# Kernel tuning notes

Hardware: AMD Instinct MI355X
Metric: run time of the kernel (lower is better)

Reference implementation:

```python
import jax, jax.numpy as jnp
import numpy as np

NS = 50000   # number of source cells
NT = 50000   # number of target cells
E = 1_600_000  # nnz of neighborhood (avg degree 32)
DIN = 64
DOUT = 64


def setup_inputs() -> dict:
    key = jax.random.key(0)
    ks = jax.random.split(key, 14)
    w_scale = ((2.0 / (DIN + DOUT)) ** 0.5) * 1.414  # xavier_uniform-ish std with gain
    a_scale = (1.0 / (3 * DOUT)) ** 0.5
    nrm = lambda k, s, sc: jax.random.normal(k, s, jnp.float32) * sc
    return {
        "x_source": jax.random.normal(ks[0], (NS, DIN), jnp.float32),
        "x_target": jax.random.normal(ks[1], (NT, DIN), jnp.float32),
        "nb_rows": jax.random.randint(ks[2], (E,), 0, NT, jnp.int32),   # target index of each nnz
        "nb_cols": jax.random.randint(ks[3], (E,), 0, NS, jnp.int32),   # source index of each nnz
        "nb_vals": jax.random.uniform(ks[4], (E,), jnp.float32),        # neighborhood values
        "cci_vals": jax.random.uniform(ks[5], (E,), jnp.float32),       # cci values (same pattern)
        "w_s": nrm(ks[6], (DIN, DOUT), w_scale),
        "w_t": nrm(ks[7], (DIN, DOUT), w_scale),
        "w_s_cci": nrm(ks[8], (DIN, DOUT), w_scale),   # shared: ParameterList([p]*2) aliases one param
        "w_t_cci": nrm(ks[9], (DIN, DOUT), w_scale),
        "src_W": nrm(ks[10], (3, 3 * DOUT, DOUT), a_scale),
        "src_b": jnp.zeros((3, DOUT), jnp.float32),
        "tgt_W": nrm(ks[11], (3, 3 * DOUT, DOUT), a_scale),
        "tgt_b": jnp.zeros((3, DOUT), jnp.float32),
    }


def _pna(seg, nbr, vals, m, W, b, n_seg):
    """PNA aggregation over a sparse neighborhood given as an edge list.
    seg: [E] destination segment ids; nbr: [E] neighbor ids into m; vals: [E] edge weights.
    Aggregators: weighted sum, mean (by neighbor count), max; then Linear(3D -> D)."""
    g = m[nbr] * vals[:, None]                                   # [E, D]
    s_sum = jax.ops.segment_sum(g, seg, num_segments=n_seg)      # [n_seg, D]
    cnt = jax.ops.segment_sum(jnp.ones_like(vals), seg, num_segments=n_seg)
    s_mean = s_sum / jnp.maximum(cnt, 1.0)[:, None]
    s_max = jax.ops.segment_max(g, seg, num_segments=n_seg)
    s_max = jnp.where(jnp.isfinite(s_max), s_max, 0.0)           # empty segments -> 0
    return jnp.concatenate([s_sum, s_mean, s_max], axis=-1) @ W + b


def reference(x_source, x_target, nb_rows, nb_cols, nb_vals, cci_vals,
              w_s, w_t, w_s_cci, w_t_cci, src_W, src_b, tgt_W, tgt_b):
    n_s, n_t = x_source.shape[0], x_target.shape[0]
    # dense projections (w_s_cci / w_t_cci are shared between the two cci branches)
    s_msg = x_source @ w_s          # [NS, DOUT]
    s_msg2 = x_source @ w_s_cci     # used for both cci branches
    t_msg = x_target @ w_t          # [NT, DOUT]
    t_msg2 = x_target @ w_t_cci
    had_vals = cci_vals * nb_vals   # sparse hadamard (same pattern)

    # message on source: aggregate target features along transposed neighborhood [NS, NT]
    msg_src = (_pna(nb_cols, nb_rows, nb_vals, t_msg, src_W[0], src_b[0], n_s)
               + _pna(nb_cols, nb_rows, cci_vals, t_msg2, src_W[1], src_b[1], n_s)
               + _pna(nb_cols, nb_rows, had_vals, t_msg2, src_W[2], src_b[2], n_s))
    # message on target: aggregate source features along neighborhood [NT, NS]
    msg_tgt = (_pna(nb_rows, nb_cols, nb_vals, s_msg, tgt_W[0], tgt_b[0], n_t)
               + _pna(nb_rows, nb_cols, cci_vals, s_msg2, tgt_W[1], tgt_b[1], n_t)
               + _pna(nb_rows, nb_cols, had_vals, s_msg2, tgt_W[2], tgt_b[2], n_t))
    # update_func is None -> return raw messages
    return msg_src, msg_tgt
```

## Files before the change

kernel.cpp:

```cpp
#include <hip/hip_runtime.h>
#include <hip/hip_bf16.h>

typedef unsigned int u32;
typedef unsigned short u16;
typedef unsigned long long u64;
typedef __attribute__((ext_vector_type(8))) short short8;
typedef __attribute__((ext_vector_type(4))) float f32x4;

__device__ __forceinline__ u32 f2bf(float f){
  u32 u = __float_as_uint(f);
  return (u + 0x7fffu + ((u >> 16) & 1u)) >> 16;
}
__device__ __forceinline__ float bflo(u32 p){ return __uint_as_float(p << 16); }
__device__ __forceinline__ float bfhi(u32 p){ return __uint_as_float(p & 0xffff0000u); }

__global__ __launch_bounds__(256) void proj_kernel(
    const float* __restrict__ xs, const float* __restrict__ xt,
    const float* __restrict__ w_s, const float* __restrict__ w_t,
    const float* __restrict__ w_s_cci, const float* __restrict__ w_t_cci,
    u32* __restrict__ mS, u32* __restrict__ mT, int ns, int nt)
{
  __shared__ float wa[4096], wb[4096];
  const int dir = blockIdx.y;
  const float* x  = dir ? xt : xs;
  const float* wA = dir ? w_t : w_s;
  const float* wB = dir ? w_t_cci : w_s_cci;
  u32* out = dir ? mT : mS;
  const int n = dir ? nt : ns;
  const int tid = threadIdx.x;
  for (int i = tid; i < 4096; i += 256){ wa[i] = wA[i]; wb[i] = wB[i]; }
  __syncthreads();
  const int wid = tid >> 6, lane = tid & 63;
  const int slice = lane >> 4, ch = lane & 15;
  for (int row = blockIdx.x*4 + wid; row < n; row += gridDim.x*4){
    float xv = x[(size_t)row*64 + lane];
    float accA = 0.f, accB = 0.f;
    #pragma unroll
    for (int k = 0; k < 64; k++){
      float xk = __shfl(xv, k, 64);
      accA = fmaf(xk, wa[k*64 + lane], accA);
      accB = fmaf(xk, wb[k*64 + lane], accB);
    }
    out[((size_t)slice*n + row)*16 + ch] = f2bf(accA) | (f2bf(accB) << 16);
  }
}

__global__ __launch_bounds__(256) void wprep_kernel(
  const float* __restrict__ srcW, const float* __restrict__ tgtW,
  u16* __restrict__ WtS, u16* __restrict__ WtT)
{
  int idx = blockIdx.x*256 + threadIdx.x;
  if (idx < 576*64){
    int col = idx / 576, k = idx - col*576;
    WtS[idx] = (u16)f2bf(srcW[(size_t)k*64 + col]);
    WtT[idx] = (u16)f2bf(tgtW[(size_t)k*64 + col]);
  }
}

__global__ __launch_bounds__(256) void hist_kernel(
  const int* __restrict__ rows, const int* __restrict__ cols,
  int* cntR, int* cntC, int E)
{
  int e = blockIdx.x*256 + threadIdx.x;
  if (e < E){
    atomicAdd(&cntR[rows[e]], 1);
    atomicAdd(&cntC[cols[e]], 1);
  }
}

__global__ __launch_bounds__(256) void scan1_kernel(
  const int* __restrict__ cntC, const int* __restrict__ cntR,
  int* __restrict__ locC, int* __restrict__ locR,
  int* __restrict__ bsum, int ns, int nt)
{
  const int arr = blockIdx.y;
  const int* cnt = arr ? cntR : cntC;
  int* loc = arr ? locR : locC;
  const int n = arr ? nt : ns;
  const int base = blockIdx.x*1024 + threadIdx.x*4;
  int v[4]; int s = 0;
  #pragma unroll
  for (int i = 0; i < 4; i++){ int idx = base+i; v[i] = (idx < n) ? cnt[idx] : 0; s += v[i]; }
  const int lane = threadIdx.x & 63, wid = threadIdx.x >> 6;
  int ps = s;
  #pragma unroll
  for (int d = 1; d < 64; d <<= 1){ int t = __shfl_up(ps, d, 64); if (lane >= d) ps += t; }
  __shared__ int wsum[4];
  if (lane == 63) wsum[wid] = ps;
  __syncthreads();
  int woff = 0;
  for (int w = 0; w < wid; w++) woff += wsum[w];
  int ex = woff + ps - s;
  #pragma unroll
  for (int i = 0; i < 4; i++){ int idx = base+i; if (idx < n) loc[idx] = ex; ex += v[i]; }
  if (threadIdx.x == 255) bsum[arr*64 + blockIdx.x] = woff + ps;
}

__global__ __launch_bounds__(128) void scan2_kernel(
  int* __restrict__ bsum, int* __restrict__ ptrC, int* __restrict__ ptrR,
  int ns, int nt)
{
  const int wid = threadIdx.x >> 6, lane = threadIdx.x & 63;
  const int n = wid ? nt : ns;
  const int nb = (n + 1023) >> 10;
  int v = (lane < nb) ? bsum[wid*64 + lane] : 0;
  int ps = v;
  #pragma unroll
  for (int d = 1; d < 64; d <<= 1){ int t = __shfl_up(ps, d, 64); if (lane >= d) ps += t; }
  if (lane < nb) bsum[wid*64 + lane] = ps - v;
  if (lane == 63){ if (wid) ptrR[nt] = ps; else ptrC[ns] = ps; }
}

__global__ __launch_bounds__(256) void scan3_kernel(
  const int* __restrict__ locC, const int* __restrict__ locR,
  const int* __restrict__ bsum,
  int* __restrict__ ptrC, int* __restrict__ ptrR,
  int* __restrict__ curC, int* __restrict__ curR, int ns, int nt)
{
  const int arr = blockIdx.y;
  const int* loc = arr ? locR : locC;
  int* ptr = arr ? ptrR : ptrC;
  int* cur = arr ? curR : curC;
  const int n = arr ? nt : ns;
  const int off = bsum[arr*64 + blockIdx.x];
  const int base = blockIdx.x*1024 + threadIdx.x;
  #pragma unroll
  for (int i = 0; i < 4; i++){
    int idx = base + i*256;
    if (idx < n){ int p = loc[idx] + off; ptr[idx] = p; cur[idx] = p; }
  }
}

__global__ __launch_bounds__(256) void scatter_kernel(
  const int* __restrict__ rows, const int* __restrict__ cols,
  const float* __restrict__ nbv, const float* __restrict__ ccv,
  int* curR, int* curC,
  int* nbrT, float* w0T, float* w1T,
  int* nbrS, float* w0S, float* w1S, int E)
{
  int e = blockIdx.x*256 + threadIdx.x;
  if (e < E){
    int r = rows[e], c = cols[e];
    float a = nbv[e], b = ccv[e];
    int pT = atomicAdd(&curR[r], 1);
    nbrT[pT] = c; w0T[pT] = a; w1T[pT] = b;
    int pS = atomicAdd(&curC[c], 1);
    nbrS[pS] = r; w0S[pS] = a; w1S[pS] = b;
  }
}

__global__ __launch_bounds__(256) void repack_kernel(
  const int* __restrict__ nbrT, const float* __restrict__ w0T, const float* __restrict__ w1T,
  const int* __restrict__ nbrS, const float* __restrict__ w0S, const float* __restrict__ w1S,
  u64* __restrict__ recT, u64* __restrict__ recS, int E)
{
  int e = blockIdx.x*256 + threadIdx.x;
  if (e < E){
    {
      float a = w0T[e], b = w1T[e];
      recT[e] = (u64)(u16)nbrT[e] | ((u64)f2bf(a) << 16) | ((u64)f2bf(b) << 32)
              | ((u64)f2bf(a*b) << 48);
    }
    {
      float a = w0S[e], b = w1S[e];
      recS[e] = (u64)(u16)nbrS[e] | ((u64)f2bf(a) << 16) | ((u64)f2bf(b) << 32)
              | ((u64)f2bf(a*b) << 48);
    }
  }
}

__global__ __launch_bounds__(256) void agg_kernel(
  const int* __restrict__ ptrC, const int* __restrict__ ptrR,
  const u64* __restrict__ recS, const u64* __restrict__ recT,
  const u32* __restrict__ mS, const u32* __restrict__ mT,
  u16* __restrict__ statsS, u16* __restrict__ statsT, int ns, int nt)
{
  const int z = blockIdx.z;
  const int dir = z >> 2, slice = z & 3;
  const int nseg = dir ? nt : ns;
  const int ntab = dir ? ns : nt;
  const int* ptr = dir ? ptrR : ptrC;
  const u64* rec = dir ? recT : recS;
  const u32* mtab = (dir ? mS : mT) + (size_t)slice*ntab*16;
  u16* stats = dir ? statsT : statsS;

  const int wid = threadIdx.x >> 6, lane = threadIdx.x & 63;
  const int seg = blockIdx.x*4 + wid;
  if (seg >= nseg) return;
  const int beg = ptr[seg], end = ptr[seg+1];
  const u32 egrp = (u32)(lane >> 4);
  const u32 chb = (u32)((lane & 15) << 2);

  float s0=0.f, s1=0.f, s2=0.f;
  float mx0=-INFINITY, mx1=-INFINITY, mx2=-INFINITY;

  const int cnt = end - beg;
  const u32 nq = (u32)(cnt >> 2);
  const u32 r  = (u32)(cnt & 3);
  u32 e = (u32)beg + egrp;

  #define GREC(i)   (rec[(size_t)(u32)(i)])
  #define GFT(p)    (*(const u32*)((const char*)mtab + (size_t)(((u32)(p) & 0xffffu)*64u + chb)))
  #define CONSUME(p, f) { \
    u32 lo_ = (u32)(p), hi_ = (u32)((p) >> 32); \
    float a_ = bfhi(lo_), b_ = bflo(hi_), ab_ = bfhi(hi_); \
    float tl_ = bflo(f), th_ = bfhi(f); \
    float g0_ = tl_*a_, g1_ = th_*b_, g2_ = th_*ab_; \
    s0 += g0_; s1 += g1_; s2 += g2_; \
    mx0 = fmaxf(mx0, g0_); mx1 = fmaxf(mx1, g1_); mx2 = fmaxf(mx2, g2_); }

  u32 k = 0;
  if (nq >= 8){
    u64 p0 = GREC(e),    p1 = GREC(e+4),  p2 = GREC(e+8),  p3 = GREC(e+12);
    u32 f0 = GFT(p0),    f1 = GFT(p1),    f2 = GFT(p2),    f3 = GFT(p3);
    u64 q0 = GREC(e+16), q1 = GREC(e+20), q2 = GREC(e+24), q3 = GREC(e+28);
    for (; k + 12 <= nq; k += 4, e += 16){
      u64 r0 = GREC(e+32), r1 = GREC(e+36), r2 = GREC(e+40), r3 = GREC(e+44);
      u32 g0 = GFT(q0), g1 = GFT(q1), g2 = GFT(q2), g3 = GFT(q3);
      CONSUME(p0, f0); CONSUME(p1, f1); CONSUME(p2, f2); CONSUME(p3, f3);
      p0=q0; p1=q1; p2=q2; p3=q3;
      f0=g0; f1=g1; f2=g2; f3=g3;
      q0=r0; q1=r1; q2=r2; q3=r3;
    }
    u32 g0 = GFT(q0), g1 = GFT(q1), g2 = GFT(q2), g3 = GFT(q3);
    CONSUME(p0, f0); CONSUME(p1, f1); CONSUME(p2, f2); CONSUME(p3, f3);
    CONSUME(q0, g0); CONSUME(q1, g1); CONSUME(q2, g2); CONSUME(q3, g3);
    k += 8; e += 32;
  }
  for (; k < nq; k++, e += 4){
    u64 p = GREC(e);
    u32 f = GFT(p);
    CONSUME(p, f);
  }
  if (egrp < r){
    u64 p = GREC((u32)beg + 4*nq + egrp);
    u32 f = GFT(p);
    CONSUME(p, f);
  }
  #undef GREC
  #undef GFT
  #undef CONSUME

  #pragma unroll
  for (int d = 16; d <= 32; d <<= 1){
    s0 += __shfl_xor(s0, d, 64);
    s1 += __shfl_xor(s1, d, 64);
    s2 += __shfl_xor(s2, d, 64);
    mx0 = fmaxf(mx0, __shfl_xor(mx0, d, 64));
    mx1 = fmaxf(mx1, __shfl_xor(mx1, d, 64));
    mx2 = fmaxf(mx2, __shfl_xor(mx2, d, 64));
  }
  if (cnt == 0){ mx0 = 0.f; mx1 = 0.f; mx2 = 0.f; }

  if (lane < 16){
    size_t base = ((size_t)slice*nseg + seg)*96 + (lane & 15);
    stats[base      ] = (u16)f2bf(s0);
    stats[base + 16 ] = (u16)f2bf(s1);
    stats[base + 32 ] = (u16)f2bf(s2);
    stats[base + 48 ] = (u16)f2bf(mx0);
    stats[base + 64 ] = (u16)f2bf(mx1);
    stats[base + 80 ] = (u16)f2bf(mx2);
  }
}

#define HROW 584

__global__ __launch_bounds__(256) void lin_kernel(
  const u16* __restrict__ statsS, const u16* __restrict__ statsT,
  const int* __restrict__ ptrC, const int* __restrict__ ptrR,
  const u16* __restrict__ WtS, const u16* __restrict__ WtT,
  const float* __restrict__ srcB, const float* __restrict__ tgtB,
  float* __restrict__ outp, int ns, int nt)
{
  __shared__ u16 h[64*HROW];
  __shared__ float invc[64];
  const int dir = blockIdx.y;
  const u16* stats = dir ? statsT : statsS;
  const int* ptr   = dir ? ptrR : ptrC;
  const u16* Wt    = dir ? WtT : WtS;
  const float* Bg  = dir ? tgtB : srcB;
  const int n = dir ? nt : ns;
  float* out = outp + (dir ? (size_t)ns*64 : 0);
  const int tid = threadIdx.x;
  const int wv = tid >> 6, lane = tid & 63;
  const int seg0 = blockIdx.x * 64;
  if (seg0 >= n) return;

  const int bcol = wv*16 + (lane & 15);
  const int krow = (lane >> 4) * 8;
  short8 bfrag[18];
  #pragma unroll
  for (int t = 0; t < 18; t++)
    bfrag[t] = *(const short8*)&Wt[(size_t)bcol*576 + t*32 + krow];

  if (tid < 64){
    int seg = seg0 + tid;
    float c = (seg < n) ? (float)(ptr[seg+1] - ptr[seg]) : 1.f;
    invc[tid] = 1.f / fmaxf(c, 1.f);
  }
  __syncthreads();

  for (int idx = tid; idx < 64*192; idx += 256){
    int s = idx / 192, i = idx - s*192;
    int blk = i >> 5, cp = (i & 31) * 2;
    int seg = seg0 + s;
    u32 v = 0;
    if (seg < n)
      v = *(const u32*)&stats[((size_t)(cp >> 4)*n + seg)*96 + blk*16 + (cp & 15)];
    u32* hrow = (u32*)&h[s*HROW];
    if (blk < 3){
      hrow[(blk*192 + cp) >> 1] = v;
      float ic = invc[s];
      hrow[(blk*192 + 64 + cp) >> 1] = f2bf(bflo(v)*ic) | (f2bf(bfhi(v)*ic) << 16);
    } else {
      hrow[((blk-3)*192 + 128 + cp) >> 1] = v;
    }
  }
  __syncthreads();

  f32x4 acc[4] = {};
  const int arow = lane & 15;
  #pragma unroll
  for (int t = 0; t < 18; t++){
    #pragma unroll
    for (int rb = 0; rb < 4; rb++){
      short8 a = *(const short8*)&h[(rb*16 + arow)*HROW + t*32 + krow];
      acc[rb] = __builtin_amdgcn_mfma_f32_16x16x32_bf16(a, bfrag[t], acc[rb], 0, 0, 0);
    }
  }

  float bv = Bg[bcol] + Bg[64 + bcol] + Bg[128 + bcol];
  #pragma unroll
  for (int rb = 0; rb < 4; rb++){
    #pragma unroll
    for (int r = 0; r < 4; r++){
      int seg = seg0 + rb*16 + (lane >> 4)*4 + r;
      if (seg < n) out[(size_t)seg*64 + bcol] = acc[rb][r] + bv;
    }
  }
}

extern "C" void kernel_launch(void* const* d_in, const int* in_sizes, int n_in,
                              void* d_out, int out_size, void* d_ws, size_t ws_size,
                              hipStream_t stream)
{
  const float* xs   = (const float*)d_in[0];
  const float* xt   = (const float*)d_in[1];
  const int*   rows = (const int*)  d_in[2];
  const int*   cols = (const int*)  d_in[3];
  const float* nbv  = (const float*)d_in[4];
  const float* ccv  = (const float*)d_in[5];
  const float* w_s  = (const float*)d_in[6];
  const float* w_t  = (const float*)d_in[7];
  const float* w_sc = (const float*)d_in[8];
  const float* w_tc = (const float*)d_in[9];
  const float* srcW = (const float*)d_in[10];
  const float* srcB = (const float*)d_in[11];
  const float* tgtW = (const float*)d_in[12];
  const float* tgtB = (const float*)d_in[13];
  const int ns = in_sizes[0] / 64;
  const int nt = in_sizes[1] / 64;
  const int E  = in_sizes[4];

  char* ws = (char*)d_ws;
  size_t off = 0;
  auto alloc = [&](size_t bytes)->char* {
    char* p = ws + off;
    off = (off + bytes + 255) & ~(size_t)255;
    return p;
  };
  u32* mS    = (u32*)alloc((size_t)ns*64*4);
  u32* mT    = (u32*)alloc((size_t)nt*64*4);
  int* cntC  = (int*)alloc((size_t)(ns+nt)*4);
  int* cntR  = cntC + ns;
  int* ptrC  = (int*)alloc((size_t)(ns+1)*4);
  int* ptrR  = (int*)alloc((size_t)(nt+1)*4);
  int* curC  = (int*)alloc((size_t)ns*4);
  int* curR  = (int*)alloc((size_t)nt*4);
  int* locC  = (int*)alloc((size_t)ns*4);
  int* locR  = (int*)alloc((size_t)nt*4);
  int* bsum  = (int*)alloc((size_t)128*4);
  int*   nbrS = (int*)  alloc((size_t)E*4);
  float* w0S  = (float*)alloc((size_t)E*4);
  float* w1S  = (float*)alloc((size_t)E*4);
  int*   nbrT = (int*)  alloc((size_t)E*4);
  float* w0T  = (float*)alloc((size_t)E*4);
  float* w1T  = (float*)alloc((size_t)E*4);
  u64* recS   = (u64*)alloc((size_t)E*8);
  u64* recT   = (u64*)alloc((size_t)E*8);
  u16* statsS = (u16*)alloc((size_t)ns*384*2);
  u16* statsT = (u16*)alloc((size_t)nt*384*2);
  u16* WtS    = (u16*)alloc((size_t)576*64*2);
  u16* WtT    = (u16*)alloc((size_t)576*64*2);

  const int mseg = (ns > nt ? ns : nt);
  const int nsb = (mseg + 1023) / 1024;

  hipMemsetAsync(cntC, 0, (size_t)(ns+nt)*4, stream);
  proj_kernel<<<dim3(128,2), 256, 0, stream>>>(xs,xt,w_s,w_t,w_sc,w_tc,mS,mT,ns,nt);
  wprep_kernel<<<(576*64 + 255)/256, 256, 0, stream>>>(srcW,tgtW,WtS,WtT);
  hist_kernel<<<(E+255)/256, 256, 0, stream>>>(rows,cols,cntR,cntC,E);
  scan1_kernel<<<dim3(nsb,2), 256, 0, stream>>>(cntC,cntR,locC,locR,bsum,ns,nt);
  scan2_kernel<<<1, 128, 0, stream>>>(bsum,ptrC,ptrR,ns,nt);
  scan3_kernel<<<dim3(nsb,2), 256, 0, stream>>>(locC,locR,bsum,ptrC,ptrR,curC,curR,ns,nt);
  scatter_kernel<<<(E+255)/256, 256, 0, stream>>>(rows,cols,nbv,ccv,curR,curC,
                                                  nbrT,w0T,w1T,nbrS,w0S,w1S,E);
  repack_kernel<<<(E+255)/256, 256, 0, stream>>>(nbrT,w0T,w1T,nbrS,w0S,w1S,
                                                 recT,recS,E);
  agg_kernel<<<dim3((mseg+3)/4, 1, 8), 256, 0, stream>>>(ptrC,ptrR,recS,recT,
                                                         mS,mT,statsS,statsT,ns,nt);
  lin_kernel<<<dim3((mseg+63)/64, 2), 256, 0, stream>>>(statsS,statsT,ptrC,ptrR,
                                                        WtS,WtT,srcB,tgtB,
                                                        (float*)d_out,ns,nt);
}
```

Measured before the change: 875.6 us.

## Merge preprocessing kernels, single-pass decoupled-lookback scan, split and simplify aggregation

Folds the weight-transpose prep into the histogram kernel and replaces the three-kernel scan with one decoupled-lookback scan that uses flag words in a zeroed state buffer. The scatter kernel now handles two edges per thread, and the aggregation kernel is split into one launch per direction, with a simpler 8-wide unrolled loop in place of the software-pipelined one. The aim is fewer launches and less intermediate traffic. The trade-offs are spin-waiting between blocks in the scan and possibly less latency hiding in the aggregation loop.

```diff
diff --git a/kernel.cpp b/kernel.cpp
--- a/kernel.cpp
+++ b/kernel.cpp
@@ -45,39 +45,41 @@
   }
 }
 
-__global__ __launch_bounds__(256) void wprep_kernel(
+__global__ __launch_bounds__(256) void hist_kernel(
+  const int* __restrict__ rows, const int* __restrict__ cols,
+  int* cntR, int* cntC, int E,
   const float* __restrict__ srcW, const float* __restrict__ tgtW,
   u16* __restrict__ WtS, u16* __restrict__ WtT)
-{
-  int idx = blockIdx.x*256 + threadIdx.x;
-  if (idx < 576*64){
-    int col = idx / 576, k = idx - col*576;
-    WtS[idx] = (u16)f2bf(srcW[(size_t)k*64 + col]);
-    WtT[idx] = (u16)f2bf(tgtW[(size_t)k*64 + col]);
-  }
-}
-
-__global__ __launch_bounds__(256) void hist_kernel(
-  const int* __restrict__ rows, const int* __restrict__ cols,
-  int* cntR, int* cntC, int E)
 {
   int e = blockIdx.x*256 + threadIdx.x;
   if (e < E){
     atomicAdd(&cntR[rows[e]], 1);
     atomicAdd(&cntC[cols[e]], 1);
   }
-}
-
-__global__ __launch_bounds__(256) void scan1_kernel(
+  if (e < 576*64){
+    int col = e / 576, k = e - col*576;
+    WtS[e] = (u16)f2bf(srcW[(size_t)k*64 + col]);
+    WtT[e] = (u16)f2bf(tgtW[(size_t)k*64 + col]);
+  }
+}
+
+__global__ __launch_bounds__(256) void scan_kernel(
   const int* __restrict__ cntC, const int* __restrict__ cntR,
-  int* __restrict__ locC, int* __restrict__ locR,
-  int* __restrict__ bsum, int ns, int nt)
+  int* __restrict__ ptrC, int* __restrict__ ptrR,
+  int* __restrict__ curC, int* __restrict__ curR,
+  u64* __restrict__ state, int ns, int nt)
 {
   const int arr = blockIdx.y;
   const int* cnt = arr ? cntR : cntC;
-  int* loc = arr ? locR : locC;
+  int* ptr = arr ? ptrR : ptrC;
+  int* cur = arr ? curR : curC;
   const int n = arr ? nt : ns;
-  const int base = blockIdx.x*1024 + threadIdx.x*4;
+  const int nb = (n + 1023) >> 10;
+  const int b = blockIdx.x;
+  if (b >= nb) return;
+  u64* st = state + arr*64;
+
+  const int base = b*1024 + threadIdx.x*4;
   int v[4]; int s = 0;
   #pragma unroll
   for (int i = 0; i < 4; i++){ int idx = base+i; v[i] = (idx < n) ? cnt[idx] : 0; s += v[i]; }
@@ -86,48 +88,40 @@
   #pragma unroll
   for (int d = 1; d < 64; d <<= 1){ int t = __shfl_up(ps, d, 64); if (lane >= d) ps += t; }
   __shared__ int wsum[4];
+  __shared__ int bloff;
   if (lane == 63) wsum[wid] = ps;
   __syncthreads();
   int woff = 0;
   for (int w = 0; w < wid; w++) woff += wsum[w];
-  int ex = woff + ps - s;
-  #pragma unroll
-  for (int i = 0; i < 4; i++){ int idx = base+i; if (idx < n) loc[idx] = ex; ex += v[i]; }
-  if (threadIdx.x == 255) bsum[arr*64 + blockIdx.x] = woff + ps;
-}
-
-__global__ __launch_bounds__(128) void scan2_kernel(
-  int* __restrict__ bsum, int* __restrict__ ptrC, int* __restrict__ ptrR,
-  int ns, int nt)
-{
-  const int wid = threadIdx.x >> 6, lane = threadIdx.x & 63;
-  const int n = wid ? nt : ns;
-  const int nb = (n + 1023) >> 10;
-  int v = (lane < nb) ? bsum[wid*64 + lane] : 0;
-  int ps = v;
-  #pragma unroll
-  for (int d = 1; d < 64; d <<= 1){ int t = __shfl_up(ps, d, 64); if (lane >= d) ps += t; }
-  if (lane < nb) bsum[wid*64 + lane] = ps - v;
-  if (lane == 63){ if (wid) ptrR[nt] = ps; else ptrC[ns] = ps; }
-}
-
-__global__ __launch_bounds__(256) void scan3_kernel(
-  const int* __restrict__ locC, const int* __restrict__ locR,
-  const int* __restrict__ bsum,
-  int* __restrict__ ptrC, int* __restrict__ ptrR,
-  int* __restrict__ curC, int* __restrict__ curR, int ns, int nt)
-{
-  const int arr = blockIdx.y;
-  const int* loc = arr ? locR : locC;
-  int* ptr = arr ? ptrR : ptrC;
-  int* cur = arr ? curR : curC;
-  const int n = arr ? nt : ns;
-  const int off = bsum[arr*64 + blockIdx.x];
-  const int base = blockIdx.x*1024 + threadIdx.x;
+  if (threadIdx.x == 0){
+    int btot = wsum[0] + wsum[1] + wsum[2] + wsum[3];
+    u64 flag1 = (b == 0) ? (2ull << 62) : (1ull << 62);
+    __hip_atomic_store(&st[b], flag1 | (u64)(u32)btot,
+                       __ATOMIC_RELEASE, __HIP_MEMORY_SCOPE_AGENT);
+    int run = 0;
+    if (b > 0){
+      int i = b - 1;
+      while (1){
+        u64 p = __hip_atomic_load(&st[i], __ATOMIC_ACQUIRE, __HIP_MEMORY_SCOPE_AGENT);
+        u64 fl = p >> 62;
+        if (fl == 0){ __builtin_amdgcn_s_sleep(1); continue; }
+        run += (int)(u32)p;
+        if (fl == 2) break;
+        i--;
+      }
+      __hip_atomic_store(&st[b], (2ull << 62) | (u64)(u32)(run + btot),
+                         __ATOMIC_RELEASE, __HIP_MEMORY_SCOPE_AGENT);
+    }
+    bloff = run;
+    if (b == nb - 1) ptr[n] = run + btot;
+  }
+  __syncthreads();
+  int ex = bloff + woff + ps - s;
   #pragma unroll
   for (int i = 0; i < 4; i++){
-    int idx = base + i*256;
-    if (idx < n){ int p = loc[idx] + off; ptr[idx] = p; cur[idx] = p; }
+    int idx = base+i;
+    if (idx < n){ ptr[idx] = ex; cur[idx] = ex; }
+    ex += v[i];
   }
 }
 
@@ -138,8 +132,19 @@
   int* nbrT, float* w0T, float* w1T,
   int* nbrS, float* w0S, float* w1S, int E)
 {
-  int e = blockIdx.x*256 + threadIdx.x;
-  if (e < E){
+  int e = (blockIdx.x*256 + threadIdx.x)*2;
+  if (e + 1 < E){
+    int r0 = rows[e], r1 = rows[e+1], c0 = cols[e], c1 = cols[e+1];
+    float a0 = nbv[e], a1 = nbv[e+1], b0 = ccv[e], b1 = ccv[e+1];
+    int pT0 = atomicAdd(&curR[r0], 1);
+    int pT1 = atomicAdd(&curR[r1], 1);
+    nbrT[pT0] = c0; w0T[pT0] = a0; w1T[pT0] = b0;
+    nbrT[pT1] = c1; w0T[pT1] = a1; w1T[pT1] = b1;
+    int pS0 = atomicAdd(&curC[c0], 1);
+    int pS1 = atomicAdd(&curC[c1], 1);
+    nbrS[pS0] = r0; w0S[pS0] = a0; w1S[pS0] = b0;
+    nbrS[pS1] = r1; w0S[pS1] = a1; w1S[pS1] = b1;
+  } else if (e < E){
     int r = rows[e], c = cols[e];
     float a = nbv[e], b = ccv[e];
     int pT = atomicAdd(&curR[r], 1);
@@ -170,26 +175,19 @@
 }
 
 __global__ __launch_bounds__(256) void agg_kernel(
-  const int* __restrict__ ptrC, const int* __restrict__ ptrR,
-  const u64* __restrict__ recS, const u64* __restrict__ recT,
-  const u32* __restrict__ mS, const u32* __restrict__ mT,
-  u16* __restrict__ statsS, u16* __restrict__ statsT, int ns, int nt)
-{
-  const int z = blockIdx.z;
-  const int dir = z >> 2, slice = z & 3;
-  const int nseg = dir ? nt : ns;
-  const int ntab = dir ? ns : nt;
-  const int* ptr = dir ? ptrR : ptrC;
-  const u64* rec = dir ? recT : recS;
-  const u32* mtab = (dir ? mS : mT) + (size_t)slice*ntab*16;
-  u16* stats = dir ? statsT : statsS;
+  const int* __restrict__ ptr, const u64* __restrict__ rec,
+  const u32* __restrict__ mtabFull, u16* __restrict__ stats,
+  int nseg, int ntab)
+{
+  const int slice = blockIdx.z;
+  const u32* mtab = mtabFull + (size_t)slice*ntab*16;
 
   const int wid = threadIdx.x >> 6, lane = threadIdx.x & 63;
   const int seg = blockIdx.x*4 + wid;
   if (seg >= nseg) return;
   const int beg = ptr[seg], end = ptr[seg+1];
   const u32 egrp = (u32)(lane >> 4);
-  const u32 chb = (u32)((lane & 15) << 2);
+  const char* mt = (const char*)mtab + ((lane & 15) << 2);
 
   float s0=0.f, s1=0.f, s2=0.f;
   float mx0=-INFINITY, mx1=-INFINITY, mx2=-INFINITY;
@@ -200,7 +198,7 @@
   u32 e = (u32)beg + egrp;
 
   #define GREC(i)   (rec[(size_t)(u32)(i)])
-  #define GFT(p)    (*(const u32*)((const char*)mtab + (size_t)(((u32)(p) & 0xffffu)*64u + chb)))
+  #define GFT(p)    (*(const u32*)(mt + (size_t)((((u32)(p) & 0xffffu) << 6))))
   #define CONSUME(p, f) { \
     u32 lo_ = (u32)(p), hi_ = (u32)((p) >> 32); \
     float a_ = bfhi(lo_), b_ = bflo(hi_), ab_ = bfhi(hi_); \
@@ -210,24 +208,20 @@
     mx0 = fmaxf(mx0, g0_); mx1 = fmaxf(mx1, g1_); mx2 = fmaxf(mx2, g2_); }
 
   u32 k = 0;
-  if (nq >= 8){
+  for (; k + 8 <= nq; k += 8, e += 32){
     u64 p0 = GREC(e),    p1 = GREC(e+4),  p2 = GREC(e+8),  p3 = GREC(e+12);
-    u32 f0 = GFT(p0),    f1 = GFT(p1),    f2 = GFT(p2),    f3 = GFT(p3);
-    u64 q0 = GREC(e+16), q1 = GREC(e+20), q2 = GREC(e+24), q3 = GREC(e+28);
-    for (; k + 12 <= nq; k += 4, e += 16){
-      u64 r0 = GREC(e+32), r1 = GREC(e+36), r2 = GREC(e+40), r3 = GREC(e+44);
-      u32 g0 = GFT(q0), g1 = GFT(q1), g2 = GFT(q2), g3 = GFT(q3);
-      CONSUME(p0, f0); CONSUME(p1, f1); CONSUME(p2, f2); CONSUME(p3, f3);
-      p0=q0; p1=q1; p2=q2; p3=q3;
-      f0=g0; f1=g1; f2=g2; f3=g3;
-      q0=r0; q1=r1; q2=r2; q3=r3;
-    }
-    u32 g0 = GFT(q0), g1 = GFT(q1), g2 = GFT(q2), g3 = GFT(q3);
+    u64 p4 = GREC(e+16), p5 = GREC(e+20), p6 = GREC(e+24), p7 = GREC(e+28);
+    u32 f0 = GFT(p0), f1 = GFT(p1), f2 = GFT(p2), f3 = GFT(p3);
+    u32 f4 = GFT(p4), f5 = GFT(p5), f6 = GFT(p6), f7 = GFT(p7);
     CONSUME(p0, f0); CONSUME(p1, f1); CONSUME(p2, f2); CONSUME(p3, f3);
-    CONSUME(q0, g0); CONSUME(q1, g1); CONSUME(q2, g2); CONSUME(q3, g3);
-    k += 8; e += 32;
-  }
-  for (; k < nq; k++, e += 4){
+    CONSUME(p4, f4); CONSUME(p5, f5); CONSUME(p6, f6); CONSUME(p7, f7);
+  }
+  for (; k + 2 <= nq; k += 2, e += 8){
+    u64 p0 = GREC(e), p1 = GREC(e+4);
+    u32 f0 = GFT(p0), f1 = GFT(p1);
+    CONSUME(p0, f0); CONSUME(p1, f1);
+  }
+  if (k < nq){
     u64 p = GREC(e);
     u32 f = GFT(p);
     CONSUME(p, f);
@@ -371,15 +365,14 @@
   };
   u32* mS    = (u32*)alloc((size_t)ns*64*4);
   u32* mT    = (u32*)alloc((size_t)nt*64*4);
-  int* cntC  = (int*)alloc((size_t)(ns+nt)*4);
+  char* zblk = alloc((size_t)(ns+nt)*4 + 1024);
+  int* cntC  = (int*)zblk;
   int* cntR  = cntC + ns;
+  u64* state = (u64*)(cntC + ns + nt);
   int* ptrC  = (int*)alloc((size_t)(ns+1)*4);
   int* ptrR  = (int*)alloc((size_t)(nt+1)*4);
   int* curC  = (int*)alloc((size_t)ns*4);
   int* curR  = (int*)alloc((size_t)nt*4);
-  int* locC  = (int*)alloc((size_t)ns*4);
-  int* locR  = (int*)alloc((size_t)nt*4);
-  int* bsum  = (int*)alloc((size_t)128*4);
   int*   nbrS = (int*)  alloc((size_t)E*4);
   float* w0S  = (float*)alloc((size_t)E*4);
   float* w1S  = (float*)alloc((size_t)E*4);
@@ -396,19 +389,18 @@
   const int mseg = (ns > nt ? ns : nt);
   const int nsb = (mseg + 1023) / 1024;
 
-  hipMemsetAsync(cntC, 0, (size_t)(ns+nt)*4, stream);
+  hipMemsetAsync(zblk, 0, (size_t)(ns+nt)*4 + 1024, stream);
   proj_kernel<<<dim3(128,2), 256, 0, stream>>>(xs,xt,w_s,w_t,w_sc,w_tc,mS,mT,ns,nt);
-  wprep_kernel<<<(576*64 + 255)/256, 256, 0, stream>>>(srcW,tgtW,WtS,WtT);
-  hist_kernel<<<(E+255)/256, 256, 0, stream>>>(rows,cols,cntR,cntC,E);
-  scan1_kernel<<<dim3(nsb,2), 256, 0, stream>>>(cntC,cntR,locC,locR,bsum,ns,nt);
-  scan2_kernel<<<1, 128, 0, stream>>>(bsum,ptrC,ptrR,ns,nt);
-  scan3_kernel<<<dim3(nsb,2), 256, 0, stream>>>(locC,locR,bsum,ptrC,ptrR,curC,curR,ns,nt);
-  scatter_kernel<<<(E+255)/256, 256, 0, stream>>>(rows,cols,nbv,ccv,curR,curC,
-                                                  nbrT,w0T,w1T,nbrS,w0S,w1S,E);
+  hist_kernel<<<(E+255)/256, 256, 0, stream>>>(rows,cols,cntR,cntC,E,
+                                               srcW,tgtW,WtS,WtT);
+  scan_kernel<<<dim3(nsb,2), 256, 0, stream>>>(cntC,cntR,ptrC,ptrR,curC,curR,
+                                               state,ns,nt);
+  scatter_kernel<<<(E/2+255)/256, 256, 0, stream>>>(rows,cols,nbv,ccv,curR,curC,
+                                                    nbrT,w0T,w1T,nbrS,w0S,w1S,E);
   repack_kernel<<<(E+255)/256, 256, 0, stream>>>(nbrT,w0T,w1T,nbrS,w0S,w1S,
                                                  recT,recS,E);
-  agg_kernel<<<dim3((mseg+3)/4, 1, 8), 256, 0, stream>>>(ptrC,ptrR,recS,recT,
-                                                         mS,mT,statsS,statsT,ns,nt);
+  agg_kernel<<<dim3((ns+3)/4, 1, 4), 256, 0, stream>>>(ptrC,recS,mT,statsS,ns,nt);
+  agg_kernel<<<dim3((nt+3)/4, 1, 4), 256, 0, stream>>>(ptrR,recT,mS,statsT,nt,ns);
   lin_kernel<<<dim3((mseg+63)/64, 2), 256, 0, stream>>>(statsS,statsT,ptrC,ptrR,
                                                         WtS,WtT,srcB,tgtB,
                                                         (float*)d_out,ns,nt);
```

After: 845.9 us. 3.4% less time.
